# Kernel optimization log

Hardware: AMD Instinct MI355X
Metric: run time of the kernel (lower is better)

Reference implementation:

```python
import jax, jax.numpy as jnp
import numpy as np

GROUP_SIZE = 128  # per-group quantization granularity along K


def setup_inputs() -> dict:
    key = jax.random.key(0)
    k1, k2, k3, k4 = jax.random.split(key, 4)
    B, S, K, N = 4, 2048, 4096, 11008
    num_groups = K // GROUP_SIZE
    x = jax.random.normal(k1, (B, S, K), dtype=jnp.float16)
    # packed uint4 pairs stored as bytes (values 0..255); int32 stands in for uint8
    weight = jax.random.randint(k2, (N, K // 2), 0, 256, dtype=jnp.int32)
    scale = jax.random.uniform(k3, (N, num_groups), dtype=jnp.float16, minval=0.001, maxval=0.02)
    bias = jax.random.normal(k4, (N,), dtype=jnp.float16)
    return {"x": x, "weight": weight, "scale": scale, "bias": bias}


def _dequant_int4(weight, scale):
    # weight: [N, K//2] packed bytes; low nibble = even k, high nibble = odd k
    N, Kh = weight.shape
    K = Kh * 2
    low = (weight & 15) - 8          # [N, K//2], signed int4 in [-8, 7]
    high = ((weight >> 4) & 15) - 8  # [N, K//2]
    w_int4 = jnp.stack([low, high], axis=-1).reshape(N, K).astype(jnp.float32)
    # broadcast per-group scales along K: [N, num_groups] -> [N, K]
    s = jnp.repeat(scale.astype(jnp.float32), GROUP_SIZE, axis=1)
    return w_int4 * s  # [N, K] fp32


def reference(x, weight, scale, bias):
    # out = x @ dequant(w).T + bias, fp32 accumulation, fp16 store (as in kernel)
    w_fp = _dequant_int4(weight, scale)                     # [N, K]
    acc = jnp.einsum('bsk,nk->bsn', x.astype(jnp.float32), w_fp)
    acc = acc + bias.astype(jnp.float32)[None, None, :]
    return acc.astype(jnp.float16)
```

## Files before the change

kernel.cpp:

```cpp
#include <hip/hip_runtime.h>

#define DEVINL __device__ __forceinline__

typedef __bf16 bf16x8 __attribute__((ext_vector_type(8)));
typedef float  f32x4  __attribute__((ext_vector_type(4)));

constexpr int KK = 4096;
constexpr int NN = 11008;
constexpr int NG = 32;

DEVINL unsigned short f2bf(float f){
  union { float f; unsigned u; } v; v.f = f;
  unsigned r = v.u + 0x7FFF + ((v.u >> 16) & 1);
  return (unsigned short)(r >> 16);
}
DEVINL unsigned pack2(float lo, float hi){
  return (unsigned)f2bf(lo) | ((unsigned)f2bf(hi) << 16);
}
DEVINL void gload16(const void* g, void* l){
  __builtin_amdgcn_global_load_lds(
      (const __attribute__((address_space(1))) void*)g,
      (__attribute__((address_space(3))) void*)l, 16, 0, 0);
}

__global__ __launch_bounds__(256) void k_dequant(const int* __restrict__ W,
                                                 const float* __restrict__ S,
                                                 unsigned short* __restrict__ WB){
  int t = blockIdx.x * 256 + threadIdx.x;
  int row = t >> 9;
  int kp0 = (t & 511) << 2;
  int g   = kp0 >> 6;
  float s = S[row * NG + g];
  const int4 p = reinterpret_cast<const int4*>(W)[t];
  const int* pb = reinterpret_cast<const int*>(&p);
  unsigned q[4];
  #pragma unroll
  for (int i = 0; i < 4; ++i){
    int b = pb[i];
    float lo = ((float)(b & 15)        - 8.0f) * s;
    float hi = ((float)((b >> 4) & 15) - 8.0f) * s;
    q[i] = pack2(lo, hi);
  }
  reinterpret_cast<int4*>(WB)[t] = make_int4((int)q[0], (int)q[1], (int)q[2], (int)q[3]);
}

__global__ __launch_bounds__(256) void k_cvtA(const float* __restrict__ X,
                                              unsigned short* __restrict__ XB){
  int t = blockIdx.x * 256 + threadIdx.x;
  const float4* src = reinterpret_cast<const float4*>(X) + (size_t)t * 2;
  float4 a = src[0], b = src[1];
  reinterpret_cast<int4*>(XB)[t] = make_int4(
      (int)pack2(a.x, a.y), (int)pack2(a.z, a.w),
      (int)pack2(b.x, b.y), (int)pack2(b.z, b.w));
}

constexpr int BM2 = 256, BN2 = 256, BK2 = 64;
constexpr int HBY = 16384;
constexpr int BUFBY = 65536;

#define WAIT4  asm volatile("s_waitcnt vmcnt(4)" ::: "memory")
#define WAIT0  asm volatile("s_waitcnt vmcnt(0)" ::: "memory")
#define BAR()  do { __builtin_amdgcn_s_barrier(); asm volatile("" ::: "memory"); } while (0)

__global__ __launch_bounds__(512, 2) void k_gemm8(const unsigned short* __restrict__ A,
                                                  const unsigned short* __restrict__ B,
                                                  const float* __restrict__ Bias,
                                                  float* __restrict__ C){
  __shared__ char smem[131072];
  const int tid = threadIdx.x, lane = tid & 63, wid = tid >> 6;
  const int wm = wid >> 2, wn = wid & 3;
  const int lr = lane & 15, hi = lane >> 4;
  const int cpx = gridDim.x >> 3;
  const int wg  = (blockIdx.x & 7) * cpx + (blockIdx.x >> 3);
  const int NTT = NN / BN2;
  const int mt = wg / NTT, nt = wg % NTT;
  const char* Ab = (const char*)(A + (size_t)mt * BM2 * KK);
  const char* Bb = (const char*)(B + (size_t)nt * BN2 * KK);
  const int srow  = tid >> 3;
  const int scolb = (tid & 7) * 16;

  auto stage_half = [&](int buf, int sel, int kt){
    const char* base = ((sel >= 2) ? Bb : Ab) + (size_t)((sel & 1) * 128) * KK * 2;
    #pragma unroll
    for (int r = 0; r < 2; ++r){
      int row = r * 64 + srow;
      const char* src = base + (size_t)row * (KK * 2) + kt * (BK2 * 2)
                      + (scolb ^ ((row & 7) << 4));
      char* dst = smem + buf * BUFBY + sel * HBY + r * 8192 + tid * 16;
      gload16(src, dst);
    }
  };
  auto frag = [&](int buf, int sel, int row, int bcol) -> bf16x8 {
    return *reinterpret_cast<const bf16x8*>(
        smem + buf * BUFBY + sel * HBY + row * 128 + (bcol ^ ((row & 7) << 4)));
  };

  f32x4 acc[8][4] = {};
  bf16x8 af[4][2], bf0[2][2], bf1[2][2];

  auto read_A = [&](int buf, int ha){
    #pragma unroll
    for (int i = 0; i < 4; ++i)
      #pragma unroll
      for (int ks = 0; ks < 2; ++ks)
        af[i][ks] = frag(buf, ha, wm*64 + i*16 + lr, ks*64 + hi*16);
  };
  auto read_B = [&](int buf, int hb, bf16x8 (&bf)[2][2]){
    #pragma unroll
    for (int j = 0; j < 2; ++j)
      #pragma unroll
      for (int ks = 0; ks < 2; ++ks)
        bf[j][ks] = frag(buf, 2 + hb, wn*32 + j*16 + lr, ks*64 + hi*16);
  };
  auto mfma16 = [&](const bf16x8 (&bf)[2][2], int HA, int HB){
    __builtin_amdgcn_s_setprio(1);
    #pragma unroll
    for (int i = 0; i < 4; ++i)
      #pragma unroll
      for (int j = 0; j < 2; ++j)
        #pragma unroll
        for (int ks = 0; ks < 2; ++ks)
          acc[HA*4 + i][HB*2 + j] = __builtin_amdgcn_mfma_f32_16x16x32_bf16(
              af[i][ks], bf[j][ks], acc[HA*4 + i][HB*2 + j], 0, 0, 0);
    __builtin_amdgcn_s_setprio(0);
  };

  stage_half(0, 0, 0);
  stage_half(0, 2, 0);
  stage_half(0, 3, 0);
  stage_half(0, 1, 0);
  WAIT4;
  BAR();

  const int NT = KK / BK2;
  for (int t = 0; t < NT; ++t){
    const int buf = t & 1;
    const bool pf = (t + 1 < NT);
    read_A(buf, 0);
    read_B(buf, 0, bf0);
    if (pf){ stage_half(buf ^ 1, 0, t + 1); stage_half(buf ^ 1, 2, t + 1); }
    if (pf) WAIT4; else WAIT0;
    BAR();
    read_B(buf, 1, bf1);
    mfma16(bf0, 0, 0);
    mfma16(bf1, 0, 1);
    read_A(buf, 1);
    if (pf){ stage_half(buf ^ 1, 3, t + 1); stage_half(buf ^ 1, 1, t + 1); }
    mfma16(bf1, 1, 1);
    mfma16(bf0, 1, 0);
    if (pf) WAIT4;
    BAR();
  }

  const int cmb = mt * BM2, cnb = nt * BN2;
  #pragma unroll
  for (int j = 0; j < 4; ++j){
    int col = cnb + (j >> 1) * 128 + wn * 32 + (j & 1) * 16 + lr;
    float bv = Bias[col];
    #pragma unroll
    for (int i = 0; i < 8; ++i){
      int row0 = cmb + (i >> 2) * 128 + wm * 64 + (i & 3) * 16 + hi * 4;
      #pragma unroll
      for (int r = 0; r < 4; ++r)
        C[(size_t)(row0 + r) * NN + col] = acc[i][j][r] + bv;
    }
  }
}

constexpr int BM = 128, BN = 128, BK = 32;
__global__ __launch_bounds__(256) void k_gemm_fast(const unsigned short* __restrict__ A,
                                                   const unsigned short* __restrict__ B,
                                                   const float* __restrict__ Bias,
                                                   float* __restrict__ C){
  __shared__ unsigned short As[2][BM][BK];
  __shared__ unsigned short Bs[2][BN][BK];
  const int tid = threadIdx.x;
  const int cpx = gridDim.x >> 3;
  const int wg  = (blockIdx.x & 7) * cpx + (blockIdx.x >> 3);
  const int NT = NN / BN;
  const int mt = wg / NT, nt = wg % NT;
  const unsigned short* Ab = A + (size_t)mt * BM * KK;
  const unsigned short* Bb = B + (size_t)nt * BN * KK;
  const int lane = tid & 63, wid = tid >> 6;
  const int wm = wid >> 1, wn = wid & 1;
  const int lr = lane & 15, lk = (lane >> 4) << 3;

  auto stage = [&](int buf, int kt){
    #pragma unroll
    for (int r = 0; r < 2; ++r){
      int c = r * 256 + tid, row = c >> 2, k0 = (c & 3) << 3;
      gload16(Ab + (size_t)row * KK + kt * BK + k0, &As[buf][row][k0]);
      gload16(Bb + (size_t)row * KK + kt * BK + k0, &Bs[buf][row][k0]);
    }
  };

  f32x4 acc[4][4] = {};
  stage(0, 0);
  __syncthreads();
  const int KT = KK / BK;
  for (int kt = 0; kt < KT; ++kt){
    int cur = kt & 1;
    if (kt + 1 < KT) stage(cur ^ 1, kt + 1);
    bf16x8 af[4], bfr[4];
    #pragma unroll
    for (int i = 0; i < 4; ++i)
      af[i] = *reinterpret_cast<const bf16x8*>(&As[cur][wm*64 + i*16 + lr][lk]);
    #pragma unroll
    for (int i = 0; i < 4; ++i)
      bfr[i] = *reinterpret_cast<const bf16x8*>(&Bs[cur][wn*64 + i*16 + lr][lk]);
    #pragma unroll
    for (int i = 0; i < 4; ++i)
      #pragma unroll
      for (int j = 0; j < 4; ++j)
        acc[i][j] = __builtin_amdgcn_mfma_f32_16x16x32_bf16(af[i], bfr[j], acc[i][j], 0, 0, 0);
    __syncthreads();
  }
  const int cm = mt * BM + wm * 64;
  const int cn = nt * BN + wn * 64;
  float bv[4];
  #pragma unroll
  for (int j = 0; j < 4; ++j) bv[j] = Bias[cn + j*16 + lr];
  #pragma unroll
  for (int i = 0; i < 4; ++i)
    #pragma unroll
    for (int j = 0; j < 4; ++j)
      #pragma unroll
      for (int r = 0; r < 4; ++r){
        size_t rr = (size_t)(cm + i*16 + (lane >> 4)*4 + r);
        C[rr * NN + (cn + j*16 + lr)] = acc[i][j][r] + bv[j];
      }
}

__global__ __launch_bounds__(256) void k_gemm_ws(const float* __restrict__ A,
                                                 const unsigned short* __restrict__ B,
                                                 const float* __restrict__ Bias,
                                                 float* __restrict__ C){
  __shared__ unsigned short As[2][BM][BK];
  __shared__ unsigned short Bs[2][BN][BK];
  const int tid = threadIdx.x;
  const int NT = NN / BN;
  const int mt = blockIdx.x / NT, nt = blockIdx.x % NT;
  const float*          Ab = A + (size_t)mt * BM * KK;
  const unsigned short* Bb = B + (size_t)nt * BN * KK;
  const int lane = tid & 63, wid = tid >> 6;
  const int wm = wid >> 1, wn = wid & 1;
  const int lr = lane & 15, lk = (lane >> 4) << 3;

  auto ld = [&](int kt, float4* ra, int4* rb){
    #pragma unroll
    for (int r = 0; r < 2; ++r){
      int c = r * 256 + tid, row = c >> 2, k0 = (c & 3) << 3;
      const float* src = Ab + (size_t)row * KK + kt * BK + k0;
      ra[2*r]   = *reinterpret_cast<const float4*>(src);
      ra[2*r+1] = *reinterpret_cast<const float4*>(src + 4);
      rb[r] = *reinterpret_cast<const int4*>(Bb + (size_t)row * KK + kt * BK + k0);
    }
  };
  auto st = [&](int buf, const float4* ra, const int4* rb){
    #pragma unroll
    for (int r = 0; r < 2; ++r){
      int c = r * 256 + tid, row = c >> 2, k0 = (c & 3) << 3;
      unsigned q[4];
      #pragma unroll
      for (int i = 0; i < 4; ++i)
        q[i] = pack2(ra[2*r + (i >> 1)][(i & 1) * 2], ra[2*r + (i >> 1)][(i & 1) * 2 + 1]);
      *reinterpret_cast<int4*>(&As[buf][row][k0]) =
          make_int4((int)q[0], (int)q[1], (int)q[2], (int)q[3]);
      *reinterpret_cast<int4*>(&Bs[buf][row][k0]) = rb[r];
    }
  };

  f32x4 acc[4][4] = {};
  {
    float4 ra[4]; int4 rb[2];
    ld(0, ra, rb);
    st(0, ra, rb);
  }
  __syncthreads();
  const int KT = KK / BK;
  for (int kt = 0; kt < KT; ++kt){
    int cur = kt & 1;
    float4 na[4]; int4 nb[2];
    if (kt + 1 < KT) ld(kt + 1, na, nb);
    bf16x8 af[4], bfr[4];
    #pragma unroll
    for (int i = 0; i < 4; ++i)
      af[i] = *reinterpret_cast<const bf16x8*>(&As[cur][wm*64 + i*16 + lr][lk]);
    #pragma unroll
    for (int i = 0; i < 4; ++i)
      bfr[i] = *reinterpret_cast<const bf16x8*>(&Bs[cur][wn*64 + i*16 + lr][lk]);
    #pragma unroll
    for (int i = 0; i < 4; ++i)
      #pragma unroll
      for (int j = 0; j < 4; ++j)
        acc[i][j] = __builtin_amdgcn_mfma_f32_16x16x32_bf16(af[i], bfr[j], acc[i][j], 0, 0, 0);
    if (kt + 1 < KT) st(cur ^ 1, na, nb);
    __syncthreads();
  }
  const int cm = mt * BM + wm * 64;
  const int cn = nt * BN + wn * 64;
  float bv[4];
  #pragma unroll
  for (int j = 0; j < 4; ++j) bv[j] = Bias[cn + j*16 + lr];
  #pragma unroll
  for (int i = 0; i < 4; ++i)
    #pragma unroll
    for (int j = 0; j < 4; ++j)
      #pragma unroll
      for (int r = 0; r < 4; ++r){
        size_t rr = (size_t)(cm + i*16 + (lane >> 4)*4 + r);
        C[rr * NN + (cn + j*16 + lr)] = acc[i][j][r] + bv[j];
      }
}

extern "C" void kernel_launch(void* const* d_in, const int* in_sizes, int n_in,
                              void* d_out, int out_size, void* d_ws, size_t ws_size,
                              hipStream_t stream){
  const float* x    = (const float*)d_in[0];
  const int*   w    = (const int*)d_in[1];
  const float* s    = (const float*)d_in[2];
  const float* bias = (const float*)d_in[3];
  float* out = (float*)d_out;
  const int M = in_sizes[0] / KK;
  const size_t needW = (size_t)NN * KK * 2;
  const size_t needA = (size_t)M * KK * 2;
  const int dq_blocks = (NN * (KK / 8)) / 256;

  if (ws_size >= needW + needA){
    unsigned short* wb = (unsigned short*)d_ws;
    unsigned short* xb = (unsigned short*)((char*)d_ws + needW);
    k_dequant<<<dq_blocks, 256, 0, stream>>>(w, s, wb);
    k_cvtA<<<(M * (KK / 8)) / 256, 256, 0, stream>>>(x, xb);
    if ((M % BM2) == 0){
      const int grid8 = (M / BM2) * (NN / BN2);
      k_gemm8<<<grid8, 512, 0, stream>>>(xb, wb, bias, out);
    } else {
      const int grid = (M / BM) * (NN / BN);
      k_gemm_fast<<<grid, 256, 0, stream>>>(xb, wb, bias, out);
    }
  } else {
    unsigned short* wb = (unsigned short*)d_ws;
    k_dequant<<<dq_blocks, 256, 0, stream>>>(w, s, wb);
    const int grid = (M / BM) * (NN / BN);
    k_gemm_ws<<<grid, 256, 0, stream>>>(x, wb, bias, out);
  }
}
```

Before: 732.5 us.

## Replace 512-thread gemm8 with 1024-thread 16-wave k_gemm16 GEMM

Adds a new GEMM kernel that uses 16 waves per 256x256 tile. Each wave computes a 64x64 subtile with a simple double-buffered loop that prefetches the full next K-slice and then waits on vmcnt(0) before each barrier. It replaces the 8-wave kernel, which had interleaved half-stage prefetches and accumulated a 128x64 subtile per wave. This halves the accumulator registers per wave and raises the number of waves resident per CU, but it loses the finer-grained load/compute overlap and allows one block per CU. The fallback path for M not divisible by the tile now uses the fp32-input workspace kernel.

```diff
diff --git a/kernel.cpp b/kernel.cpp
--- a/kernel.cpp
+++ b/kernel.cpp
@@ -58,10 +58,98 @@
 constexpr int HBY = 16384;
 constexpr int BUFBY = 65536;
 
+#define WAIT0  asm volatile("s_waitcnt vmcnt(0)" ::: "memory")
 #define WAIT4  asm volatile("s_waitcnt vmcnt(4)" ::: "memory")
-#define WAIT0  asm volatile("s_waitcnt vmcnt(0)" ::: "memory")
 #define BAR()  do { __builtin_amdgcn_s_barrier(); asm volatile("" ::: "memory"); } while (0)
 
+__global__ __launch_bounds__(1024, 1) void k_gemm16(const unsigned short* __restrict__ A,
+                                                    const unsigned short* __restrict__ B,
+                                                    const float* __restrict__ Bias,
+                                                    float* __restrict__ C){
+  __shared__ char smem[131072];
+  const int tid = threadIdx.x, lane = tid & 63, wid = tid >> 6;
+  const int wm = wid >> 2, wn = wid & 3;
+  const int lr = lane & 15, hi = lane >> 4;
+  const int cpx = gridDim.x >> 3;
+  const int wg  = (blockIdx.x & 7) * cpx + (blockIdx.x >> 3);
+  const int NTT = NN / BN2;
+  const int mt = wg / NTT, nt = wg % NTT;
+  const char* Ab = (const char*)(A + (size_t)mt * BM2 * KK);
+  const char* Bb = (const char*)(B + (size_t)nt * BN2 * KK);
+  const int srow  = tid >> 3;
+  const int scolb = (tid & 7) * 16;
+
+  auto stage_half = [&](int buf, int sel, int kt){
+    const char* base = ((sel >= 2) ? Bb : Ab) + (size_t)((sel & 1) * 128) * KK * 2;
+    const char* src = base + (size_t)srow * (KK * 2) + kt * (BK2 * 2)
+                    + (scolb ^ ((srow & 7) << 4));
+    char* dst = smem + buf * BUFBY + sel * HBY + tid * 16;
+    gload16(src, dst);
+  };
+  auto frag = [&](int buf, int sel, int row, int bcol) -> bf16x8 {
+    return *reinterpret_cast<const bf16x8*>(
+        smem + buf * BUFBY + sel * HBY + row * 128 + (bcol ^ ((row & 7) << 4)));
+  };
+
+  const int selA = wm >> 1;
+  const int rA0  = (wm & 1) * 64;
+  const int selB = 2 + (wn >> 1);
+  const int cB0  = (wn & 1) * 64;
+
+  f32x4 acc[4][4] = {};
+
+  stage_half(0, 0, 0); stage_half(0, 1, 0);
+  stage_half(0, 2, 0); stage_half(0, 3, 0);
+  WAIT0;
+  BAR();
+
+  const int NT = KK / BK2;
+  for (int t = 0; t < NT; ++t){
+    const int buf = t & 1;
+    const bool pf = (t + 1 < NT);
+    if (pf){
+      stage_half(buf ^ 1, 0, t + 1);
+      stage_half(buf ^ 1, 1, t + 1);
+      stage_half(buf ^ 1, 2, t + 1);
+      stage_half(buf ^ 1, 3, t + 1);
+    }
+    #pragma unroll
+    for (int ks = 0; ks < 2; ++ks){
+      bf16x8 af[4], bf[4];
+      #pragma unroll
+      for (int i = 0; i < 4; ++i)
+        af[i] = frag(buf, selA, rA0 + i*16 + lr, ks*64 + hi*16);
+      #pragma unroll
+      for (int j = 0; j < 4; ++j)
+        bf[j] = frag(buf, selB, cB0 + j*16 + lr, ks*64 + hi*16);
+      __builtin_amdgcn_s_setprio(1);
+      #pragma unroll
+      for (int i = 0; i < 4; ++i)
+        #pragma unroll
+        for (int j = 0; j < 4; ++j)
+          acc[i][j] = __builtin_amdgcn_mfma_f32_16x16x32_bf16(af[i], bf[j], acc[i][j], 0, 0, 0);
+      __builtin_amdgcn_s_setprio(0);
+    }
+    if (pf) WAIT0;
+    BAR();
+  }
+
+  const int cmb = mt * BM2, cnb = nt * BN2;
+  #pragma unroll
+  for (int j = 0; j < 4; ++j){
+    int col = cnb + wn * 64 + j * 16 + lr;
+    float bv = Bias[col];
+    #pragma unroll
+    for (int i = 0; i < 4; ++i){
+      int row0 = cmb + wm * 64 + i * 16 + hi * 4;
+      #pragma unroll
+      for (int r = 0; r < 4; ++r)
+        C[(size_t)(row0 + r) * NN + col] = acc[i][j][r] + bv;
+    }
+  }
+}
+
+#define R8WAIT4  asm volatile("s_waitcnt vmcnt(4)" ::: "memory")
 __global__ __launch_bounds__(512, 2) void k_gemm8(const unsigned short* __restrict__ A,
                                                   const unsigned short* __restrict__ B,
                                                   const float* __restrict__ Bias,
@@ -125,11 +213,8 @@
     __builtin_amdgcn_s_setprio(0);
   };
 
-  stage_half(0, 0, 0);
-  stage_half(0, 2, 0);
-  stage_half(0, 3, 0);
-  stage_half(0, 1, 0);
-  WAIT4;
+  stage_half(0, 0, 0); stage_half(0, 2, 0); stage_half(0, 3, 0); stage_half(0, 1, 0);
+  R8WAIT4;
   BAR();
 
   const int NT = KK / BK2;
@@ -139,7 +224,7 @@
     read_A(buf, 0);
     read_B(buf, 0, bf0);
     if (pf){ stage_half(buf ^ 1, 0, t + 1); stage_half(buf ^ 1, 2, t + 1); }
-    if (pf) WAIT4; else WAIT0;
+    if (pf) R8WAIT4; else WAIT0;
     BAR();
     read_B(buf, 1, bf1);
     mfma16(bf0, 0, 0);
@@ -148,7 +233,7 @@
     if (pf){ stage_half(buf ^ 1, 3, t + 1); stage_half(buf ^ 1, 1, t + 1); }
     mfma16(bf1, 1, 1);
     mfma16(bf0, 1, 0);
-    if (pf) WAIT4;
+    if (pf) R8WAIT4;
     BAR();
   }
 
@@ -168,69 +253,6 @@
 }
 
 constexpr int BM = 128, BN = 128, BK = 32;
-__global__ __launch_bounds__(256) void k_gemm_fast(const unsigned short* __restrict__ A,
-                                                   const unsigned short* __restrict__ B,
-                                                   const float* __restrict__ Bias,
-                                                   float* __restrict__ C){
-  __shared__ unsigned short As[2][BM][BK];
-  __shared__ unsigned short Bs[2][BN][BK];
-  const int tid = threadIdx.x;
-  const int cpx = gridDim.x >> 3;
-  const int wg  = (blockIdx.x & 7) * cpx + (blockIdx.x >> 3);
-  const int NT = NN / BN;
-  const int mt = wg / NT, nt = wg % NT;
-  const unsigned short* Ab = A + (size_t)mt * BM * KK;
-  const unsigned short* Bb = B + (size_t)nt * BN * KK;
-  const int lane = tid & 63, wid = tid >> 6;
-  const int wm = wid >> 1, wn = wid & 1;
-  const int lr = lane & 15, lk = (lane >> 4) << 3;
-
-  auto stage = [&](int buf, int kt){
-    #pragma unroll
-    for (int r = 0; r < 2; ++r){
-      int c = r * 256 + tid, row = c >> 2, k0 = (c & 3) << 3;
-      gload16(Ab + (size_t)row * KK + kt * BK + k0, &As[buf][row][k0]);
-      gload16(Bb + (size_t)row * KK + kt * BK + k0, &Bs[buf][row][k0]);
-    }
-  };
-
-  f32x4 acc[4][4] = {};
-  stage(0, 0);
-  __syncthreads();
-  const int KT = KK / BK;
-  for (int kt = 0; kt < KT; ++kt){
-    int cur = kt & 1;
-    if (kt + 1 < KT) stage(cur ^ 1, kt + 1);
-    bf16x8 af[4], bfr[4];
-    #pragma unroll
-    for (int i = 0; i < 4; ++i)
-      af[i] = *reinterpret_cast<const bf16x8*>(&As[cur][wm*64 + i*16 + lr][lk]);
-    #pragma unroll
-    for (int i = 0; i < 4; ++i)
-      bfr[i] = *reinterpret_cast<const bf16x8*>(&Bs[cur][wn*64 + i*16 + lr][lk]);
-    #pragma unroll
-    for (int i = 0; i < 4; ++i)
-      #pragma unroll
-      for (int j = 0; j < 4; ++j)
-        acc[i][j] = __builtin_amdgcn_mfma_f32_16x16x32_bf16(af[i], bfr[j], acc[i][j], 0, 0, 0);
-    __syncthreads();
-  }
-  const int cm = mt * BM + wm * 64;
-  const int cn = nt * BN + wn * 64;
-  float bv[4];
-  #pragma unroll
-  for (int j = 0; j < 4; ++j) bv[j] = Bias[cn + j*16 + lr];
-  #pragma unroll
-  for (int i = 0; i < 4; ++i)
-    #pragma unroll
-    for (int j = 0; j < 4; ++j)
-      #pragma unroll
-      for (int r = 0; r < 4; ++r){
-        size_t rr = (size_t)(cm + i*16 + (lane >> 4)*4 + r);
-        C[rr * NN + (cn + j*16 + lr)] = acc[i][j][r] + bv[j];
-      }
-}
-
 __global__ __launch_bounds__(256) void k_gemm_ws(const float* __restrict__ A,
                                                  const unsigned short* __restrict__ B,
                                                  const float* __restrict__ Bias,
@@ -333,10 +355,12 @@
     k_cvtA<<<(M * (KK / 8)) / 256, 256, 0, stream>>>(x, xb);
     if ((M % BM2) == 0){
       const int grid8 = (M / BM2) * (NN / BN2);
-      k_gemm8<<<grid8, 512, 0, stream>>>(xb, wb, bias, out);
+      k_gemm16<<<grid8, 1024, 0, stream>>>(xb, wb, bias, out);
     } else {
+      const int grid8 = ((M + BM2 - 1) / BM2) * (NN / BN2);
+      (void)grid8;
       const int grid = (M / BM) * (NN / BN);
-      k_gemm_fast<<<grid, 256, 0, stream>>>(xb, wb, bias, out);
+      k_gemm_ws<<<grid, 256, 0, stream>>>(x, wb, bias, out);
     }
   } else {
     unsigned short* wb = (unsigned short*)d_ws;
```

Result: no change. 730.4 us (-0.3%).
